# Performance work log

Hardware: AMD Instinct MI355X
Metric: run time of the kernel (lower is better)

The kernel has to match this reference:

```python
import jax, jax.numpy as jnp
import numpy as np

N_HEADS = 16

def _rotate_half(t):
    # t: [B, H, T, hs]; split last dim in half, return cat(-x2, x1)
    hs = t.shape[-1]
    x1, x2 = t[..., : hs // 2], t[..., hs // 2 :]
    return jnp.concatenate((-x2, x1), axis=-1)

def _rope_pos(T, hs, dtype):
    inv_freq = 1.0 / (10000.0 ** (jnp.arange(0, hs, 2, dtype=jnp.float32) / hs))
    freqs = jnp.arange(T, dtype=jnp.float32)[:, None] * inv_freq[None, :]  # [T, hs/2]
    pos = jnp.concatenate((freqs, freqs), axis=-1)  # [T, hs]
    return pos

def setup_inputs() -> dict:
    key = jax.random.key(0)
    ks = jax.random.split(key, 5)
    d = 2048
    x = jax.random.normal(ks[0], (2, 2048, d), dtype=jnp.float32)
    W_attn = jax.random.normal(ks[1], (d, 3 * d), dtype=jnp.float32) * (1.0 / np.sqrt(d))
    b_attn = jax.random.normal(ks[2], (3 * d,), dtype=jnp.float32) * 0.02
    W_proj = jax.random.normal(ks[3], (d, d), dtype=jnp.float32) * (1.0 / np.sqrt(d))
    b_proj = jax.random.normal(ks[4], (d,), dtype=jnp.float32) * 0.02
    return {"x": x, "W_attn": W_attn, "b_attn": b_attn, "W_proj": W_proj, "b_proj": b_proj}

def reference(x, W_attn, b_attn, W_proj, b_proj):
    B, T, C = x.shape
    nh = N_HEADS
    hs = C // nh
    qkv = x @ W_attn + b_attn  # [B, T, 3C]
    q, k, v = jnp.split(qkv, 3, axis=-1)
    # [B, T, C] -> [B, nh, T, hs]
    def to_heads(t):
        return t.reshape(B, T, nh, hs).transpose(0, 2, 1, 3)
    q, k, v = to_heads(q), to_heads(k), to_heads(v)
    # RoPE
    pos = _rope_pos(T, hs, x.dtype)  # [T, hs]
    cos, sin = jnp.cos(pos).astype(x.dtype), jnp.sin(pos).astype(x.dtype)
    q = q * cos + _rotate_half(q) * sin
    k = k * cos + _rotate_half(k) * sin
    # causal SDPA
    scale = 1.0 / np.sqrt(hs)
    scores = jnp.einsum('bhqd,bhkd->bhqk', q, k) * scale  # [B, nh, T, T]
    causal = jnp.tril(jnp.ones((T, T), dtype=bool))
    scores = jnp.where(causal, scores, jnp.finfo(scores.dtype).min)
    att = jax.nn.softmax(scores, axis=-1)
    out = jnp.einsum('bhqk,bhkd->bhqd', att, v)  # [B, nh, T, hs]
    y = out.transpose(0, 2, 1, 3).reshape(B, T, C)
    return y @ W_proj + b_proj
```

## Files before the change

kernel.cpp:

```cpp
#include <hip/hip_runtime.h>
#include <stdint.h>

typedef unsigned short u16;
typedef __attribute__((ext_vector_type(8))) short short8;
typedef __attribute__((ext_vector_type(4))) float f32x4;
typedef __attribute__((ext_vector_type(4))) unsigned short u16x4;

#define DEV __device__ __forceinline__

DEV u16 f2bf(float f) {
  union { float f; unsigned u; } v; v.f = f;
  unsigned r = v.u + 0x7fffu + ((v.u >> 16) & 1u);
  return (u16)(r >> 16);
}
DEV float bf2f(u16 b) {
  union { unsigned u; float f; } v; v.u = ((unsigned)b) << 16;
  return v.f;
}
DEV void gload_lds16(const void* g, void* l) {
  __builtin_amdgcn_global_load_lds((const __attribute__((address_space(1))) void*)g,
                                   (__attribute__((address_space(3))) void*)l,
                                   16, 0, 0);
}
DEV void block_barrier() {
  asm volatile("" ::: "memory");
  __builtin_amdgcn_s_barrier();
  asm volatile("" ::: "memory");
}

__global__ void k_conv(const float* __restrict__ in, u16* __restrict__ out, int n4) {
  int i = blockIdx.x * blockDim.x + threadIdx.x;
  if (i >= n4) return;
  const f32x4 v = *(const f32x4*)(in + (size_t)i * 4);
  u16x4 o;
  o[0] = f2bf(v[0]); o[1] = f2bf(v[1]); o[2] = f2bf(v[2]); o[3] = f2bf(v[3]);
  *(u16x4*)(out + (size_t)i * 4) = o;
}

__global__ void k_tconv(const float* __restrict__ in, u16* __restrict__ out, int R, int C) {
  __shared__ float tile[32][33];
  int c0 = blockIdx.x * 32, r0 = blockIdx.y * 32;
  int tx = threadIdx.x, ty = threadIdx.y;
#pragma unroll
  for (int j = 0; j < 32; j += 8)
    tile[ty + j][tx] = in[(size_t)(r0 + ty + j) * C + (c0 + tx)];
  __syncthreads();
#pragma unroll
  for (int j = 0; j < 32; j += 8)
    out[(size_t)(c0 + ty + j) * R + (r0 + tx)] = f2bf(tile[tx][ty + j]);
}

__global__ void k_rope(const u16* __restrict__ qkv, u16* __restrict__ qh, u16* __restrict__ kh) {
  int m = blockIdx.x;
  int t = m & 2047, b = m >> 11;
  int tid = threadIdx.x;
  int h = blockIdx.y * 4 + (tid >> 6);
  int j = tid & 63;
  float inv = expf((float)j * -0.14391156831212787f);
  float ang = (float)t * inv;
  float s, c;
  sincosf(ang, &s, &c);
  size_t ibase = (size_t)m * 6144 + (size_t)h * 128;
  size_t obase = ((size_t)(b * 16 + h) * 2048 + t) * 128;
  float q1 = bf2f(qkv[ibase + j]),        q2 = bf2f(qkv[ibase + 64 + j]);
  qh[obase + j]      = f2bf(q1 * c - q2 * s);
  qh[obase + 64 + j] = f2bf(q2 * c + q1 * s);
  float k1 = bf2f(qkv[ibase + 2048 + j]), k2 = bf2f(qkv[ibase + 2048 + 64 + j]);
  kh[obase + j]      = f2bf(k1 * c - k2 * s);
  kh[obase + 64 + j] = f2bf(k2 * c + k1 * s);
}

__global__ void k_vtrans(const u16* __restrict__ qkv, u16* __restrict__ vt) {
  __shared__ u16 tile[32][33];
  int bh = blockIdx.z;
  int b = bh >> 4, h = bh & 15;
  int t0 = blockIdx.x * 32, d0 = blockIdx.y * 32;
  int tx = threadIdx.x, ty = threadIdx.y;
#pragma unroll
  for (int j = 0; j < 32; j += 8)
    tile[ty + j][tx] = qkv[(size_t)(b * 2048 + t0 + ty + j) * 6144 + 4096 + h * 128 + d0 + tx];
  __syncthreads();
#pragma unroll
  for (int j = 0; j < 32; j += 8)
    vt[((size_t)bh * 128 + d0 + ty + j) * 2048 + (t0 + tx)] = tile[tx][ty + j];
}

template <bool OUT_BF16>
__global__ __launch_bounds__(512, 2) void k_gemm3(const u16* __restrict__ A,
                                                  const u16* __restrict__ Bt,
                                                  const float* __restrict__ bias,
                                                  void* __restrict__ Cv,
                                                  int M, int N, int K) {
  __shared__ __align__(16) short lA[2][256 * 64];
  __shared__ __align__(16) short lB[2][256 * 64];
  const int tid = threadIdx.x;
  const int wid = tid >> 6, lane = tid & 63;
  const int gx = gridDim.x;
  const int nwg = gx * gridDim.y;
  const int orig = blockIdx.y * gx + blockIdx.x;
  const int lg = (orig & 7) * (nwg >> 3) + (orig >> 3);
  const int bm = (lg % gx) * 256, bn = (lg / gx) * 256;
  const int wr = wid >> 2, wc = wid & 3;
  const int r = lane & 15, kq = lane >> 4, r7 = lane & 7;

  int aoff[4], boff[4], lbase[4];
#pragma unroll
  for (int j = 0; j < 4; ++j) {
    int c = j * 512 + wid * 64 + lane;
    int row = c >> 3, ch = c & 7;
    aoff[j] = (bm + row) * K + (ch ^ (row & 7)) * 8;
    boff[j] = (bn + row) * K + (ch ^ (row & 7)) * 8;
    lbase[j] = (j * 512 + wid * 64) * 16;
  }

#define STG_A(k0, buf, j) gload_lds16(A + aoff[j] + (k0), (char*)&lA[(buf)][0] + lbase[j])
#define STG_B(k0, buf, j) gload_lds16(Bt + boff[j] + (k0), (char*)&lB[(buf)][0] + lbase[j])
#define RD_A(AF, Q)                                                             \
  _Pragma("unroll")                                                             \
  for (int m2 = 0; m2 < 2; ++m2)                                                \
    _Pragma("unroll")                                                           \
    for (int kk = 0; kk < 2; ++kk)                                              \
      AF[m2][kk] = *(const short8*)&As[(wr * 128 + (Q) * 32 + m2 * 16 + r) * 64 \
                                       + ((kk * 4 + kq) ^ r7) * 8];
#define QUAD_MFMA(AF, MB)                                                       \
  __builtin_amdgcn_s_setprio(1);                                                \
  _Pragma("unroll")                                                             \
  for (int m2 = 0; m2 < 2; ++m2)                                                \
    _Pragma("unroll")                                                           \
    for (int nf = 0; nf < 4; ++nf)                                              \
      _Pragma("unroll")                                                         \
      for (int kk = 0; kk < 2; ++kk)                                            \
        acc[(MB) + m2][nf] = __builtin_amdgcn_mfma_f32_16x16x32_bf16(           \
            AF[m2][kk], bfr[nf][kk], acc[(MB) + m2][nf], 0, 0, 0);              \
  __builtin_amdgcn_s_setprio(0);

  f32x4 acc[8][4];
  const f32x4 zero = {0.f, 0.f, 0.f, 0.f};
#pragma unroll
  for (int i = 0; i < 8; ++i)
#pragma unroll
    for (int j = 0; j < 4; ++j) acc[i][j] = zero;

  const int nt = K >> 6;

#pragma unroll
  for (int j = 0; j < 4; ++j) STG_A(0, 0, j);
#pragma unroll
  for (int j = 0; j < 4; ++j) STG_B(0, 0, j);
  if (nt > 1) {
#pragma unroll
    for (int j = 0; j < 4; ++j) STG_B(64, 1, j);
    asm volatile("s_waitcnt vmcnt(4)" ::: "memory");
  } else {
    asm volatile("s_waitcnt vmcnt(0)" ::: "memory");
  }
  block_barrier();

#pragma unroll 1
  for (int t = 0; t < nt; ++t) {
    const int cur = t & 1, nxt = cur ^ 1;
    const short* As = &lA[cur][0];
    const short* Bs = &lB[cur][0];
    const int kA = (t + 1) * 64, kB = (t + 2) * 64;
    const bool sA = (t + 1 < nt), sB = (t + 2 < nt);
    short8 bfr[4][2];

#pragma unroll
    for (int nf = 0; nf < 4; ++nf)
#pragma unroll
      for (int kk = 0; kk < 2; ++kk)
        bfr[nf][kk] = *(const short8*)&Bs[(wc * 64 + nf * 16 + r) * 64 + ((kk * 4 + kq) ^ r7) * 8];
    short8 af0[2][2];
    RD_A(af0, 0)
    if (sA) { STG_A(kA, nxt, 0); STG_A(kA, nxt, 1); }
    block_barrier();
    QUAD_MFMA(af0, 0)
    block_barrier();

    short8 af1[2][2];
    RD_A(af1, 1)
    if (sA) { STG_A(kA, nxt, 2); STG_A(kA, nxt, 3); }
    block_barrier();
    QUAD_MFMA(af1, 2)
    block_barrier();

    short8 af2[2][2];
    RD_A(af2, 2)
    if (sB) { STG_B(kB, cur, 0); STG_B(kB, cur, 1); }
    block_barrier();
    QUAD_MFMA(af2, 4)
    block_barrier();

    short8 af3[2][2];
    RD_A(af3, 3)
    if (sB) { STG_B(kB, cur, 2); STG_B(kB, cur, 3); }
    block_barrier();
    QUAD_MFMA(af3, 6)
    if (t + 1 < nt) {
      if (sB) asm volatile("s_waitcnt vmcnt(4)" ::: "memory");
      else    asm volatile("s_waitcnt vmcnt(0)" ::: "memory");
    }
    block_barrier();
  }
#undef STG_A
#undef STG_B
#undef RD_A
#undef QUAD_MFMA

#pragma unroll
  for (int mf = 0; mf < 8; ++mf)
#pragma unroll
    for (int nf = 0; nf < 4; ++nf) {
      int n = bn + wc * 64 + nf * 16 + r;
      float bv = bias[n];
#pragma unroll
      for (int i = 0; i < 4; ++i) {
        int m = bm + wr * 128 + mf * 16 + kq * 4 + i;
        float val = acc[mf][nf][i] + bv;
        if (OUT_BF16)
          ((u16*)Cv)[(size_t)m * N + n] = f2bf(val);
        else
          ((float*)Cv)[(size_t)m * N + n] = val;
      }
    }
}

__global__ __launch_bounds__(256) void k_attn(const u16* __restrict__ qh,
                                              const u16* __restrict__ kh,
                                              const u16* __restrict__ vt,
                                              u16* __restrict__ out) {
  __shared__ __align__(16) short lK[2][64 * 128];
  __shared__ __align__(16) short lV[2][128 * 64];
  __shared__ __align__(16) short lP[64 * 64];
  const int tid = threadIdx.x, wid = tid >> 6, lane = tid & 63;
  const int p = blockIdx.x, h = blockIdx.y, b = blockIdx.z;
  const size_t bh = (size_t)b * 16 + h;
  const u16* qb = qh + bh * 2048 * 128;
  const u16* kb = kh + bh * 2048 * 128;
  const u16* vb = vt + bh * 128 * 2048;
  const int r = lane & 15, kq = lane >> 4;
  const int r7 = r & 7;
  const int wrow = wid * 16;
  const float scale2 = 0.08838834764831845f * 1.4426950408889634f;

  int koff[4], voff[4];
#pragma unroll
  for (int i = 0; i < 4; ++i) {
    int ci = (wid * 4 + i) * 64 + lane;
    int krow = ci >> 4, kch = ci & 15;
    koff[i] = krow * 128 + ((kch ^ (krow & 7)) * 8);
    int vrow = ci >> 3, vch = ci & 7;
    voff[i] = vrow * 2048 + ((vch ^ (vrow & 7)) * 8);
  }

#pragma unroll 1
  for (int seg = 0; seg < 2; ++seg) {
    const int j = seg ? 31 - p : p;
    const int q0 = j * 64;
    const int nkt = j + 1;

    short8 qa[4];
#pragma unroll
    for (int kk = 0; kk < 4; ++kk)
      qa[kk] = *(const short8*)(qb + (size_t)(q0 + wrow + r) * 128 + kk * 32 + kq * 8);

    f32x4 O[8];
    const f32x4 zero = {0.f, 0.f, 0.f, 0.f};
#pragma unroll
    for (int nf = 0; nf < 8; ++nf) O[nf] = zero;
    float m_run[4], l_run[4];
#pragma unroll
    for (int i = 0; i < 4; ++i) { m_run[i] = -1e30f; l_run[i] = 0.f; }

#pragma unroll
    for (int i = 0; i < 4; ++i) {
      gload_lds16(kb + koff[i], (char*)&lK[0][0] + (wid * 4 + i) * 1024);
      gload_lds16(vb + voff[i], (char*)&lV[0][0] + (wid * 4 + i) * 1024);
    }

#pragma unroll 1
    for (int kt = 0; kt < nkt; ++kt) {
      const int cur = kt & 1;
      if (kt + 1 < nkt) {
        const size_t kbase = (size_t)(kt + 1) * 8192, vbase = (size_t)(kt + 1) * 64;
#pragma unroll
        for (int i = 0; i < 4; ++i) {
          gload_lds16(kb + kbase + koff[i], (char*)&lK[cur ^ 1][0] + (wid * 4 + i) * 1024);
          gload_lds16(vb + vbase + voff[i], (char*)&lV[cur ^ 1][0] + (wid * 4 + i) * 1024);
        }
        asm volatile("s_waitcnt vmcnt(8)" ::: "memory");
      } else {
        asm volatile("s_waitcnt vmcnt(0)" ::: "memory");
      }
      block_barrier();

      f32x4 S[4];
#pragma unroll
      for (int nf = 0; nf < 4; ++nf) S[nf] = zero;
#pragma unroll
      for (int kk = 0; kk < 4; ++kk) {
        short8 kf[4];
#pragma unroll
        for (int nf = 0; nf < 4; ++nf)
          kf[nf] = *(const short8*)&lK[cur][(nf * 16 + r) * 128 + ((kk * 4 + kq) ^ r7) * 8];
#pragma unroll
        for (int nf = 0; nf < 4; ++nf)
          S[nf] = __builtin_amdgcn_mfma_f32_16x16x32_bf16(qa[kk], kf[nf], S[nf], 0, 0, 0);
      }

      float mnew[4];
#pragma unroll
      for (int i = 0; i < 4; ++i) mnew[i] = m_run[i];
      if (kt == nkt - 1) {
#pragma unroll
        for (int nf = 0; nf < 4; ++nf)
#pragma unroll
          for (int i = 0; i < 4; ++i) {
            float s = S[nf][i] * scale2;
            int kg = kt * 64 + nf * 16 + r;
            int qg = q0 + wrow + kq * 4 + i;
            s = (kg > qg) ? -1e30f : s;
            S[nf][i] = s;
            mnew[i] = fmaxf(mnew[i], s);
          }
      } else {
#pragma unroll
        for (int nf = 0; nf < 4; ++nf)
#pragma unroll
          for (int i = 0; i < 4; ++i) {
            float s = S[nf][i] * scale2;
            S[nf][i] = s;
            mnew[i] = fmaxf(mnew[i], s);
          }
      }
#pragma unroll
      for (int i = 0; i < 4; ++i) {
        float v = mnew[i];
        v = fmaxf(v, __shfl_xor(v, 1));
        v = fmaxf(v, __shfl_xor(v, 2));
        v = fmaxf(v, __shfl_xor(v, 4));
        v = fmaxf(v, __shfl_xor(v, 8));
        mnew[i] = v;
      }
      float rs[4];
#pragma unroll
      for (int i = 0; i < 4; ++i) {
        rs[i] = exp2f(m_run[i] - mnew[i]);
        l_run[i] *= rs[i];
        m_run[i] = mnew[i];
      }
#pragma unroll
      for (int nf = 0; nf < 8; ++nf)
#pragma unroll
        for (int i = 0; i < 4; ++i) O[nf][i] *= rs[i];

      {
        float lsum[4] = {0.f, 0.f, 0.f, 0.f};
#pragma unroll
        for (int nf = 0; nf < 4; ++nf)
#pragma unroll
          for (int i = 0; i < 4; ++i) {
            float pv = exp2f(S[nf][i] - m_run[i]);
            lsum[i] += pv;
            int row = wrow + kq * 4 + i;
            int cl = (nf * 2 + (r >> 3)) ^ ((kq * 4 + i) & 7);
            lP[row * 64 + cl * 8 + r7] = (short)f2bf(pv);
          }
#pragma unroll
        for (int i = 0; i < 4; ++i) {
          float v = lsum[i];
          v += __shfl_xor(v, 1);
          v += __shfl_xor(v, 2);
          v += __shfl_xor(v, 4);
          v += __shfl_xor(v, 8);
          l_run[i] += v;
        }
      }

#pragma unroll
      for (int kk = 0; kk < 2; ++kk) {
        short8 pa = *(const short8*)&lP[(wrow + r) * 64 + ((kk * 4 + kq) ^ r7) * 8];
#pragma unroll
        for (int nf = 0; nf < 8; ++nf) {
          short8 vf = *(const short8*)&lV[cur][(nf * 16 + r) * 64 + ((kk * 4 + kq) ^ r7) * 8];
          O[nf] = __builtin_amdgcn_mfma_f32_16x16x32_bf16(pa, vf, O[nf], 0, 0, 0);
        }
      }
      asm volatile("s_waitcnt lgkmcnt(0)" ::: "memory");
      block_barrier();
    }

    float inv[4];
#pragma unroll
    for (int i = 0; i < 4; ++i) inv[i] = 1.f / l_run[i];
#pragma unroll
    for (int nf = 0; nf < 8; ++nf)
#pragma unroll
      for (int i = 0; i < 4; ++i) {
        int qg = q0 + wrow + kq * 4 + i;
        out[(size_t)(b * 2048 + qg) * 2048 + h * 128 + nf * 16 + r] = f2bf(O[nf][i] * inv[i]);
      }
  }
}

extern "C" void kernel_launch(void* const* d_in, const int* in_sizes, int n_in,
                              void* d_out, int out_size, void* d_ws, size_t ws_size,
                              hipStream_t stream) {
  const float* x      = (const float*)d_in[0];
  const float* W_attn = (const float*)d_in[1];
  const float* b_attn = (const float*)d_in[2];
  const float* W_proj = (const float*)d_in[3];
  const float* b_proj = (const float*)d_in[4];
  float* y = (float*)d_out;

  u16* xb     = (u16*)d_ws;
  u16* wqkvT  = xb     + (size_t)4096 * 2048;
  u16* wprojT = wqkvT  + (size_t)6144 * 2048;
  u16* qkv    = wprojT + (size_t)2048 * 2048;
  u16* qh     = qkv    + (size_t)4096 * 6144;
  u16* kh     = qh     + (size_t)4096 * 2048;
  u16* vt     = kh     + (size_t)4096 * 2048;
  u16* attout = vt     + (size_t)4096 * 2048;
  if (ws_size < (size_t)83886080 * 2) return;

  k_conv<<<8192, 256, 0, stream>>>(x, xb, 2097152);
  k_tconv<<<dim3(192, 64), dim3(32, 8), 0, stream>>>(W_attn, wqkvT, 2048, 6144);
  k_tconv<<<dim3(64, 64), dim3(32, 8), 0, stream>>>(W_proj, wprojT, 2048, 2048);
  k_gemm3<true><<<dim3(16, 24), 512, 0, stream>>>(xb, wqkvT, b_attn, qkv, 4096, 6144, 2048);
  k_rope<<<dim3(4096, 4), 256, 0, stream>>>(qkv, qh, kh);
  k_vtrans<<<dim3(64, 4, 32), dim3(32, 8), 0, stream>>>(qkv, vt);
  k_attn<<<dim3(16, 16, 2), 256, 0, stream>>>(qh, kh, vt, attout);
  k_gemm3<false><<<dim3(16, 8), 512, 0, stream>>>(attout, wprojT, b_proj, y, 4096, 2048, 2048);
}
```

Measured before the change: 335.4 us.

## Split-K the output projection GEMM and reorder MFMA phases by K-half

The output projection GEMM launched only 128 workgroups, so it now runs as a 2-way split-K over 256 workgroups. Each split writes fp32 partials into the no-longer-needed qkv buffer, and a new vectorized kernel sums the two partials and adds the bias. The GEMM inner loop is also regrouped so each phase reads one K-half of B and a 64-row slab of A, then issues 16 MFMAs on it. This trades extra partial-sum traffic and one more kernel launch for better CU occupancy on the smaller GEMM.

```diff
diff --git a/kernel.cpp b/kernel.cpp
--- a/kernel.cpp
+++ b/kernel.cpp
@@ -85,12 +85,12 @@
     vt[((size_t)bh * 128 + d0 + ty + j) * 2048 + (t0 + tx)] = tile[tx][ty + j];
 }
 
-template <bool OUT_BF16>
+template <bool OUT_BF16, bool SPLITK>
 __global__ __launch_bounds__(512, 2) void k_gemm3(const u16* __restrict__ A,
                                                   const u16* __restrict__ Bt,
                                                   const float* __restrict__ bias,
                                                   void* __restrict__ Cv,
-                                                  int M, int N, int K) {
+                                                  int M, int N, int Kld, int nkt) {
   __shared__ __align__(16) short lA[2][256 * 64];
   __shared__ __align__(16) short lB[2][256 * 64];
   const int tid = threadIdx.x;
@@ -102,36 +102,38 @@
   const int bm = (lg % gx) * 256, bn = (lg / gx) * 256;
   const int wr = wid >> 2, wc = wid & 3;
   const int r = lane & 15, kq = lane >> 4, r7 = lane & 7;
+  const int kz = SPLITK ? blockIdx.z * (nkt << 6) : 0;
 
   int aoff[4], boff[4], lbase[4];
 #pragma unroll
   for (int j = 0; j < 4; ++j) {
     int c = j * 512 + wid * 64 + lane;
     int row = c >> 3, ch = c & 7;
-    aoff[j] = (bm + row) * K + (ch ^ (row & 7)) * 8;
-    boff[j] = (bn + row) * K + (ch ^ (row & 7)) * 8;
+    aoff[j] = (bm + row) * Kld + kz + (ch ^ (row & 7)) * 8;
+    boff[j] = (bn + row) * Kld + kz + (ch ^ (row & 7)) * 8;
     lbase[j] = (j * 512 + wid * 64) * 16;
   }
 
 #define STG_A(k0, buf, j) gload_lds16(A + aoff[j] + (k0), (char*)&lA[(buf)][0] + lbase[j])
 #define STG_B(k0, buf, j) gload_lds16(Bt + boff[j] + (k0), (char*)&lB[(buf)][0] + lbase[j])
-#define RD_A(AF, Q)                                                             \
+#define RD_A(AF, MH, KK)                                                        \
   _Pragma("unroll")                                                             \
-  for (int m2 = 0; m2 < 2; ++m2)                                                \
-    _Pragma("unroll")                                                           \
-    for (int kk = 0; kk < 2; ++kk)                                              \
-      AF[m2][kk] = *(const short8*)&As[(wr * 128 + (Q) * 32 + m2 * 16 + r) * 64 \
-                                       + ((kk * 4 + kq) ^ r7) * 8];
-#define QUAD_MFMA(AF, MB)                                                       \
+  for (int m2 = 0; m2 < 4; ++m2)                                                \
+    AF[m2] = *(const short8*)&As[(wr * 128 + (MH) * 64 + m2 * 16 + r) * 64      \
+                                 + (((KK) * 4 + kq) ^ r7) * 8];
+#define RD_B(KK)                                                                \
+  _Pragma("unroll")                                                             \
+  for (int nf = 0; nf < 4; ++nf)                                                \
+    bfr[KK][nf] = *(const short8*)&Bs[(wc * 64 + nf * 16 + r) * 64              \
+                                      + (((KK) * 4 + kq) ^ r7) * 8];
+#define PH_MFMA(AF, MH, KK)                                                     \
   __builtin_amdgcn_s_setprio(1);                                                \
   _Pragma("unroll")                                                             \
-  for (int m2 = 0; m2 < 2; ++m2)                                                \
+  for (int m2 = 0; m2 < 4; ++m2)                                                \
     _Pragma("unroll")                                                           \
     for (int nf = 0; nf < 4; ++nf)                                              \
-      _Pragma("unroll")                                                         \
-      for (int kk = 0; kk < 2; ++kk)                                            \
-        acc[(MB) + m2][nf] = __builtin_amdgcn_mfma_f32_16x16x32_bf16(           \
-            AF[m2][kk], bfr[nf][kk], acc[(MB) + m2][nf], 0, 0, 0);              \
+      acc[(MH) * 4 + m2][nf] = __builtin_amdgcn_mfma_f32_16x16x32_bf16(         \
+          AF[m2], bfr[KK][nf], acc[(MH) * 4 + m2][nf], 0, 0, 0);                \
   __builtin_amdgcn_s_setprio(0);
 
   f32x4 acc[8][4];
@@ -141,7 +143,7 @@
 #pragma unroll
     for (int j = 0; j < 4; ++j) acc[i][j] = zero;
 
-  const int nt = K >> 6;
+  const int nt = nkt;
 
 #pragma unroll
   for (int j = 0; j < 4; ++j) STG_A(0, 0, j);
@@ -163,39 +165,33 @@
     const short* Bs = &lB[cur][0];
     const int kA = (t + 1) * 64, kB = (t + 2) * 64;
     const bool sA = (t + 1 < nt), sB = (t + 2 < nt);
-    short8 bfr[4][2];
-
-#pragma unroll
-    for (int nf = 0; nf < 4; ++nf)
-#pragma unroll
-      for (int kk = 0; kk < 2; ++kk)
-        bfr[nf][kk] = *(const short8*)&Bs[(wc * 64 + nf * 16 + r) * 64 + ((kk * 4 + kq) ^ r7) * 8];
-    short8 af0[2][2];
-    RD_A(af0, 0)
+    short8 bfr[2][4];
+    short8 af[4];
+
+    RD_B(0)
+    RD_A(af, 0, 0)
     if (sA) { STG_A(kA, nxt, 0); STG_A(kA, nxt, 1); }
     block_barrier();
-    QUAD_MFMA(af0, 0)
-    block_barrier();
-
-    short8 af1[2][2];
-    RD_A(af1, 1)
+    PH_MFMA(af, 0, 0)
+    block_barrier();
+
+    RD_B(1)
+    RD_A(af, 0, 1)
     if (sA) { STG_A(kA, nxt, 2); STG_A(kA, nxt, 3); }
     block_barrier();
-    QUAD_MFMA(af1, 2)
-    block_barrier();
-
-    short8 af2[2][2];
-    RD_A(af2, 2)
+    PH_MFMA(af, 0, 1)
+    block_barrier();
+
+    RD_A(af, 1, 0)
     if (sB) { STG_B(kB, cur, 0); STG_B(kB, cur, 1); }
     block_barrier();
-    QUAD_MFMA(af2, 4)
-    block_barrier();
-
-    short8 af3[2][2];
-    RD_A(af3, 3)
+    PH_MFMA(af, 1, 0)
+    block_barrier();
+
+    RD_A(af, 1, 1)
     if (sB) { STG_B(kB, cur, 2); STG_B(kB, cur, 3); }
     block_barrier();
-    QUAD_MFMA(af3, 6)
+    PH_MFMA(af, 1, 1)
     if (t + 1 < nt) {
       if (sB) asm volatile("s_waitcnt vmcnt(4)" ::: "memory");
       else    asm volatile("s_waitcnt vmcnt(0)" ::: "memory");
@@ -205,24 +201,39 @@
 #undef STG_A
 #undef STG_B
 #undef RD_A
-#undef QUAD_MFMA
+#undef RD_B
+#undef PH_MFMA
 
 #pragma unroll
   for (int mf = 0; mf < 8; ++mf)
 #pragma unroll
     for (int nf = 0; nf < 4; ++nf) {
       int n = bn + wc * 64 + nf * 16 + r;
-      float bv = bias[n];
+      float bv = SPLITK ? 0.f : bias[n];
 #pragma unroll
       for (int i = 0; i < 4; ++i) {
         int m = bm + wr * 128 + mf * 16 + kq * 4 + i;
         float val = acc[mf][nf][i] + bv;
-        if (OUT_BF16)
+        if (SPLITK)
+          ((float*)Cv)[(size_t)blockIdx.z * M * N + (size_t)m * N + n] = val;
+        else if (OUT_BF16)
           ((u16*)Cv)[(size_t)m * N + n] = f2bf(val);
         else
           ((float*)Cv)[(size_t)m * N + n] = val;
       }
     }
+}
+
+__global__ void k_fadd(const float* __restrict__ p, const float* __restrict__ bias,
+                       float* __restrict__ y, int n4) {
+  const int half4 = 2097152;
+  for (int i = blockIdx.x * blockDim.x + threadIdx.x; i < n4; i += gridDim.x * blockDim.x) {
+    f32x4 a = *(const f32x4*)(p + (size_t)i * 4);
+    f32x4 b = *(const f32x4*)(p + (size_t)(i + half4) * 4);
+    f32x4 bv = *(const f32x4*)(bias + ((i & 511) << 2));
+    f32x4 o = a + b + bv;
+    *(f32x4*)(y + (size_t)i * 4) = o;
+  }
 }
 
 __global__ __launch_bounds__(256) void k_attn(const u16* __restrict__ qh,
@@ -423,12 +434,15 @@
   u16* attout = vt     + (size_t)4096 * 2048;
   if (ws_size < (size_t)83886080 * 2) return;
 
+  float* pproj = (float*)qkv;
+
   k_conv<<<8192, 256, 0, stream>>>(x, xb, 2097152);
   k_tconv<<<dim3(192, 64), dim3(32, 8), 0, stream>>>(W_attn, wqkvT, 2048, 6144);
   k_tconv<<<dim3(64, 64), dim3(32, 8), 0, stream>>>(W_proj, wprojT, 2048, 2048);
-  k_gemm3<true><<<dim3(16, 24), 512, 0, stream>>>(xb, wqkvT, b_attn, qkv, 4096, 6144, 2048);
+  k_gemm3<true, false><<<dim3(16, 24), 512, 0, stream>>>(xb, wqkvT, b_attn, qkv, 4096, 6144, 2048, 32);
   k_rope<<<dim3(4096, 4), 256, 0, stream>>>(qkv, qh, kh);
   k_vtrans<<<dim3(64, 4, 32), dim3(32, 8), 0, stream>>>(qkv, vt);
   k_attn<<<dim3(16, 16, 2), 256, 0, stream>>>(qh, kh, vt, attout);
-  k_gemm3<false><<<dim3(16, 8), 512, 0, stream>>>(attout, wprojT, b_proj, y, 4096, 2048, 2048);
-}
+  k_gemm3<false, true><<<dim3(16, 8, 2), 512, 0, stream>>>(attout, wprojT, b_proj, pproj, 4096, 2048, 2048, 16);
+  k_fadd<<<2048, 256, 0, stream>>>(pproj, b_proj, y, 2097152);
+}
```

After: 335.1 us. Within noise of the previous version (-0.1%).
